# Kernel tuning notes

Hardware: AMD Instinct MI355X
Metric: run time of the kernel (lower is better)

## Reference

```python
import jax, jax.numpy as jnp
import numpy as np

N, E, H, D, FE = 50000, 400000, 4, 64, 64  # nodes, edges, heads, per-head dim, edge feat dim
NEG_SLOPE = 0.2


def setup_inputs() -> dict:
    key = jax.random.key(0)
    ks = jax.random.split(key, 18)
    def p(k, shape, s=0.1):
        return jax.random.normal(k, shape, dtype=jnp.float32) * s
    return dict(
        features=p(ks[0], (N, D), 1.0),
        edge_feat=p(ks[1], (E, FE), 1.0),
        src=jax.random.randint(ks[2], (E,), 0, N),
        dst=jax.random.randint(ks[3], (E,), 0, N),
        # layer 0: in=64 -> H*D=256, residual Linear since 64 != 256
        W0=p(ks[4], (D, H * D)), We0=p(ks[5], (FE, H * D)),
        al0=p(ks[6], (H, D)), ar0=p(ks[7], (H, D)), ae0=p(ks[8], (H, D)),
        b0=p(ks[9], (H * D,)), Wres0=p(ks[10], (D, H * D)),
        # layer 1 (last): in=256 -> H*D=256, residual = identity view
        W1=p(ks[11], (H * D, H * D)), We1=p(ks[12], (FE, H * D)),
        al1=p(ks[13], (H, D)), ar1=p(ks[14], (H, D)), ae1=p(ks[15], (H, D)),
        b1=p(ks[16], (H * D,)),
    )


def _edge_gat_layer(h, ef, src, dst, W, We, al, ar, ae, b, Wres=None):
    n = h.shape[0]
    ft = (h @ W).reshape(n, H, D)          # (N,H,D) projected node feats
    fe = (ef @ We).reshape(-1, H, D)       # (E,H,D) projected edge feats
    el = jnp.sum(ft * al, axis=-1)         # (N,H)
    er = jnp.sum(ft * ar, axis=-1)         # (N,H)
    ee = jnp.sum(fe * ae, axis=-1)         # (E,H)
    e = el[src] + er[dst] + ee             # (E,H)
    e = jnp.where(e > 0, e, NEG_SLOPE * e)  # leaky_relu(0.2)
    # segment softmax over incoming edges of each dst node
    m = jax.ops.segment_max(jax.lax.stop_gradient(e), dst, num_segments=n)
    ex = jnp.exp(e - m[dst])
    den = jax.ops.segment_sum(ex, dst, num_segments=n)
    a = ex / den[dst]                      # (E,H) attention
    out = jax.ops.segment_sum(ft[src] * a[:, :, None], dst, num_segments=n)  # (N,H,D)
    res = (h @ Wres).reshape(n, H, D) if Wres is not None else h.reshape(n, H, D)
    return out + res + b.reshape(1, H, D)


def reference(features, edge_feat, src, dst,
              W0, We0, al0, ar0, ae0, b0, Wres0,
              W1, We1, al1, ar1, ae1, b1):
    h = _edge_gat_layer(features, edge_feat, src, dst, W0, We0, al0, ar0, ae0, b0, Wres0)
    h = jax.nn.elu(h.reshape(N, H * D))    # flatten heads + ELU between layers
    h = _edge_gat_layer(h, edge_feat, src, dst, W1, We1, al1, ar1, ae1, b1)
    return h.mean(axis=1)                  # (N, D) mean over heads on last layer
```

## Files before the change

kernel.cpp:

```cpp
#include <hip/hip_runtime.h>
#include <hip/hip_bf16.h>

#define NN 50000
#define EE 400000
#define NB 196

typedef __bf16 bf16_8 __attribute__((ext_vector_type(8)));
typedef float f32x4 __attribute__((ext_vector_type(4)));

__global__ __launch_bounds__(256) void prep_kernel(
    const float* __restrict__ features, __bf16* __restrict__ fbf,
    const float* __restrict__ W0, const float* __restrict__ Wres0, __bf16* __restrict__ Bt0,
    const float* __restrict__ W1, __bf16* __restrict__ Bt1,
    const float* __restrict__ We0, const float* __restrict__ ae0, float* __restrict__ Ve0,
    const float* __restrict__ We1, const float* __restrict__ ae1, float* __restrict__ Ve1,
    const int* __restrict__ dst, int* __restrict__ cnt) {
  int b = blockIdx.x;
  int t = threadIdx.x;
  if (b < 1563) {
    int i = b * 256 + t;
    if (i < NN * 64 / 8) {
      const float4* p = (const float4*)features + (size_t)i * 2;
      float4 a = p[0], c = p[1];
      bf16_8 v = {(__bf16)a.x, (__bf16)a.y, (__bf16)a.z, (__bf16)a.w,
                  (__bf16)c.x, (__bf16)c.y, (__bf16)c.z, (__bf16)c.w};
      *(bf16_8*)(fbf + (size_t)i * 8) = v;
    }
  } else if (b < 1563 + 128) {
    int idx = (b - 1563) * 256 + t;
    int j = idx >> 6, k = idx & 63;
    float v = (j < 256) ? W0[k * 256 + j] : Wres0[k * 256 + (j - 256)];
    Bt0[idx] = (__bf16)v;
  } else if (b < 1563 + 128 + 256) {
    int idx = (b - 1563 - 128) * 256 + t;
    int j = idx >> 8, k = idx & 255;
    Bt1[idx] = (__bf16)W1[k * 256 + j];
  } else if (b == 1947) {
    int f = t >> 2, h = t & 3;
    float s = 0.f;
    for (int d = 0; d < 64; ++d) s += We0[f * 256 + h * 64 + d] * ae0[h * 64 + d];
    Ve0[f * 4 + h] = s;
  } else if (b == 1948) {
    int f = t >> 2, h = t & 3;
    float s = 0.f;
    for (int d = 0; d < 64; ++d) s += We1[f * 256 + h * 64 + d] * ae1[h * 64 + d];
    Ve1[f * 4 + h] = s;
  } else {
    int e = (b - 1949) * 256 + t;
    if (e < EE) atomicAdd(&cnt[dst[e]], 1);
  }
}

__global__ __launch_bounds__(256) void scan1_kernel(const int* __restrict__ cnt,
                                                    int* __restrict__ scanbuf,
                                                    int* __restrict__ blocksum) {
  __shared__ int s[256];
  int t = threadIdx.x;
  int idx = blockIdx.x * 256 + t;
  int c = (idx < NN) ? cnt[idx] : 0;
  s[t] = c;
  __syncthreads();
  for (int d = 1; d < 256; d <<= 1) {
    int v = (t >= d) ? s[t - d] : 0;
    __syncthreads();
    s[t] += v;
    __syncthreads();
  }
  if (idx < NN) scanbuf[idx] = s[t];
  if (t == 255) blocksum[blockIdx.x] = s[255];
}

__global__ __launch_bounds__(256) void scan2_kernel(const int* __restrict__ blocksum,
                                                    int* __restrict__ blockoff, int nb) {
  __shared__ int s[256];
  int t = threadIdx.x;
  int c = (t < nb) ? blocksum[t] : 0;
  s[t] = c;
  __syncthreads();
  for (int d = 1; d < 256; d <<= 1) {
    int v = (t >= d) ? s[t - d] : 0;
    __syncthreads();
    s[t] += v;
    __syncthreads();
  }
  if (t < nb) blockoff[t] = s[t] - c;
}

__global__ __launch_bounds__(256) void scan3_kernel(const int* __restrict__ scanbuf,
                                                    const int* __restrict__ cnt,
                                                    const int* __restrict__ blockoff,
                                                    int* __restrict__ off,
                                                    int* __restrict__ cur) {
  int idx = blockIdx.x * 256 + threadIdx.x;
  if (idx < NN) {
    int o = blockoff[blockIdx.x] + scanbuf[idx] - cnt[idx];
    off[idx] = o;
    cur[idx] = o;
  }
  if (idx == 0) off[NN] = EE;
}

__global__ __launch_bounds__(256) void fill_kernel(const int* __restrict__ src,
                                                   const int* __restrict__ dst,
                                                   int* __restrict__ cur,
                                                   int* __restrict__ srcc,
                                                   int* __restrict__ eidc) {
  int e = blockIdx.x * 256 + threadIdx.x;
  if (e < EE) {
    int p = atomicAdd(&cur[dst[e]], 1);
    srcc[p] = src[e];
    eidc[p] = e;
  }
}

__global__ __launch_bounds__(256) void eek_kernel(const float* __restrict__ ef,
                                                  const float* __restrict__ Ve0,
                                                  const float* __restrict__ Ve1,
                                                  float* __restrict__ eeo) {
  __shared__ float V0[256], V1[256];
  V0[threadIdx.x] = Ve0[threadIdx.x];
  V1[threadIdx.x] = Ve1[threadIdx.x];
  __syncthreads();
  int r = threadIdx.x >> 2, sub = threadIdx.x & 3;
  int e = blockIdx.x * 64 + r;
  if (e >= EE) return;
  float a0 = 0, a1 = 0, a2 = 0, a3 = 0;
  float c0 = 0, c1 = 0, c2 = 0, c3 = 0;
  const float* row = ef + (size_t)e * 64 + sub * 16;
#pragma unroll
  for (int i = 0; i < 16; i += 4) {
    float4 v = *(const float4*)(row + i);
    float xs[4] = {v.x, v.y, v.z, v.w};
#pragma unroll
    for (int j = 0; j < 4; ++j) {
      float x = xs[j];
      int idx = (sub * 16 + i + j) * 4;
      a0 += x * V0[idx + 0]; a1 += x * V0[idx + 1];
      a2 += x * V0[idx + 2]; a3 += x * V0[idx + 3];
      c0 += x * V1[idx + 0]; c1 += x * V1[idx + 1];
      c2 += x * V1[idx + 2]; c3 += x * V1[idx + 3];
    }
  }
#pragma unroll
  for (int o = 1; o < 4; o <<= 1) {
    a0 += __shfl_xor(a0, o); a1 += __shfl_xor(a1, o);
    a2 += __shfl_xor(a2, o); a3 += __shfl_xor(a3, o);
    c0 += __shfl_xor(c0, o); c1 += __shfl_xor(c1, o);
    c2 += __shfl_xor(c2, o); c3 += __shfl_xor(c3, o);
  }
  if (sub == 0) {
    float4 u; u.x = a0; u.y = a1; u.z = a2; u.w = a3;
    float4 w; w.x = c0; w.y = c1; w.z = c2; w.w = c3;
    *(float4*)(eeo + (size_t)e * 8) = u;
    *(float4*)(eeo + (size_t)e * 8 + 4) = w;
  }
}

#define LDK 40
__global__ __launch_bounds__(256) void gemm_kernel(const __bf16* __restrict__ A,
                                                   const __bf16* __restrict__ Bt,
                                                   __bf16* __restrict__ ft,
                                                   __bf16* __restrict__ base,
                                                   const float* __restrict__ bias,
                                                   const float* __restrict__ al,
                                                   const float* __restrict__ ar,
                                                   float* __restrict__ el,
                                                   float* __restrict__ er,
                                                   int M, int K) {
  __shared__ __align__(16) __bf16 Al[64 * LDK];
  __shared__ __align__(16) __bf16 Bl[64 * LDK];
  int tid = threadIdx.x;
  int wav = tid >> 6, lane = tid & 63;
  int quad = lane >> 4, l16 = lane & 15;
  int bm = blockIdx.x * 64;
  int bn = blockIdx.y * 64;
  int sr = tid >> 2;
  int sk = (tid & 3) << 3;

  f32x4 acc[4] = {{0, 0, 0, 0}, {0, 0, 0, 0}, {0, 0, 0, 0}, {0, 0, 0, 0}};

  for (int k0 = 0; k0 < K; k0 += 32) {
    uint4 av = {0, 0, 0, 0};
    int arow = bm + sr;
    if (arow < M) av = *(const uint4*)(A + (size_t)arow * K + k0 + sk);
    uint4 bv = *(const uint4*)(Bt + (size_t)(bn + sr) * K + k0 + sk);
    __syncthreads();
    *(uint4*)&Al[sr * LDK + sk] = av;
    *(uint4*)&Bl[sr * LDK + sk] = bv;
    __syncthreads();
    bf16_8 af = *(const bf16_8*)&Al[(wav * 16 + l16) * LDK + quad * 8];
#pragma unroll
    for (int nt = 0; nt < 4; ++nt) {
      bf16_8 bf = *(const bf16_8*)&Bl[(nt * 16 + l16) * LDK + quad * 8];
      acc[nt] = __builtin_amdgcn_mfma_f32_16x16x32_bf16(af, bf, acc[nt], 0, 0, 0);
    }
  }

  int row0 = bm + wav * 16 + quad * 4;

  if (bn < 256) {
    int hb = bn >> 6;
#pragma unroll
    for (int r = 0; r < 4; ++r) {
      float pl = 0.f, pr = 0.f;
#pragma unroll
      for (int nt = 0; nt < 4; ++nt) {
        float v = acc[nt][r];
        int d = nt * 16 + l16;
        pl += v * al[hb * 64 + d];
        pr += v * ar[hb * 64 + d];
      }
#pragma unroll
      for (int o2 = 8; o2 > 0; o2 >>= 1) {
        pl += __shfl_xor(pl, o2);
        pr += __shfl_xor(pr, o2);
      }
      int row = row0 + r;
      if (l16 == 0 && row < M) {
        el[row * 4 + hb] = pl;
        er[row * 4 + hb] = pr;
      }
    }
  }

#pragma unroll
  for (int nt = 0; nt < 4; ++nt) {
    int col = bn + nt * 16 + l16;
#pragma unroll
    for (int r = 0; r < 4; ++r) {
      int row = row0 + r;
      if (row < M) {
        float v = acc[nt][r];
        if (col < 256)
          ft[(size_t)row * 256 + col] = (__bf16)v;
        else
          base[(size_t)row * 256 + (col - 256)] = (__bf16)(v + bias[col - 256]);
      }
    }
  }
}

template <int LAYER>
__global__ __launch_bounds__(256) void agg_kernel(const int* __restrict__ off,
                                                  const int* __restrict__ srcc,
                                                  const int* __restrict__ eidc,
                                                  const float* __restrict__ eeo,
                                                  const float* __restrict__ el,
                                                  const float* __restrict__ er,
                                                  const __bf16* __restrict__ ft,
                                                  const __bf16* prev,
                                                  const float* __restrict__ bias,
                                                  __bf16* outb,
                                                  float* __restrict__ outf) {
  __shared__ float red[256];
  int n = blockIdx.x;
  int t = threadIdx.x, h = t >> 6, lane = t & 63;
  int beg = off[n], end = off[n + 1];
  float pv = (float)prev[(size_t)n * 256 + t];
  float bv = (LAYER == 1) ? bias[t] : 0.f;
  float ern = er[n * 4 + h];
  int offd = h * 64 + lane;

  float acc = 0.f, den = 0.f;
  int j = beg;
  for (; j + 4 <= end; j += 4) {
    int s0 = srcc[j], s1 = srcc[j + 1], s2 = srcc[j + 2], s3 = srcc[j + 3];
    int e0 = eidc[j], e1 = eidc[j + 1], e2 = eidc[j + 2], e3 = eidc[j + 3];
    float z0 = el[s0 * 4 + h] + ern + eeo[(size_t)e0 * 8 + LAYER * 4 + h];
    float z1 = el[s1 * 4 + h] + ern + eeo[(size_t)e1 * 8 + LAYER * 4 + h];
    float z2 = el[s2 * 4 + h] + ern + eeo[(size_t)e2 * 8 + LAYER * 4 + h];
    float z3 = el[s3 * 4 + h] + ern + eeo[(size_t)e3 * 8 + LAYER * 4 + h];
    float w0 = __expf(z0 > 0.f ? z0 : 0.2f * z0);
    float w1 = __expf(z1 > 0.f ? z1 : 0.2f * z1);
    float w2 = __expf(z2 > 0.f ? z2 : 0.2f * z2);
    float w3 = __expf(z3 > 0.f ? z3 : 0.2f * z3);
    float v0 = (float)ft[(size_t)s0 * 256 + offd];
    float v1 = (float)ft[(size_t)s1 * 256 + offd];
    float v2 = (float)ft[(size_t)s2 * 256 + offd];
    float v3 = (float)ft[(size_t)s3 * 256 + offd];
    acc += w0 * v0; acc += w1 * v1; acc += w2 * v2; acc += w3 * v3;
    den += w0 + w1 + w2 + w3;
  }
  for (; j < end; ++j) {
    int s = srcc[j];
    float z = el[s * 4 + h] + ern + eeo[(size_t)eidc[j] * 8 + LAYER * 4 + h];
    float w = __expf(z > 0.f ? z : 0.2f * z);
    acc += w * (float)ft[(size_t)s * 256 + offd];
    den += w;
  }
  float res = (end > beg) ? acc / den : 0.f;

  if (LAYER == 0) {
    float v = res + pv;
    v = v > 0.f ? v : (__expf(v) - 1.0f);
    outb[(size_t)n * 256 + t] = (__bf16)v;
  } else {
    red[t] = res + pv + bv;
    __syncthreads();
    if (t < 64)
      outf[(size_t)n * 64 + t] =
          0.25f * (red[t] + red[t + 64] + red[t + 128] + red[t + 192]);
  }
}

extern "C" void kernel_launch(void* const* d_in, const int* in_sizes, int n_in,
                              void* d_out, int out_size, void* d_ws, size_t ws_size,
                              hipStream_t stream) {
  const float* features  = (const float*)d_in[0];
  const float* edge_feat = (const float*)d_in[1];
  const int*   src       = (const int*)d_in[2];
  const int*   dst       = (const int*)d_in[3];
  const float* W0    = (const float*)d_in[4];
  const float* We0   = (const float*)d_in[5];
  const float* al0   = (const float*)d_in[6];
  const float* ar0   = (const float*)d_in[7];
  const float* ae0   = (const float*)d_in[8];
  const float* b0    = (const float*)d_in[9];
  const float* Wres0 = (const float*)d_in[10];
  const float* W1    = (const float*)d_in[11];
  const float* We1   = (const float*)d_in[12];
  const float* al1   = (const float*)d_in[13];
  const float* ar1   = (const float*)d_in[14];
  const float* ae1   = (const float*)d_in[15];
  const float* b1    = (const float*)d_in[16];
  float* out = (float*)d_out;

  char* ws = (char*)d_ws;
  size_t o = 0;
  auto alloc = [&](size_t bytes) {
    void* p = ws + o;
    o = (o + bytes + 255) & ~(size_t)255;
    return p;
  };
  int*    cnt      = (int*)alloc((size_t)NN * 4);
  int*    scanbuf  = (int*)alloc((size_t)NN * 4);
  int*    blocksum = (int*)alloc(256 * 4);
  int*    blockoff = (int*)alloc(256 * 4);
  int*    off      = (int*)alloc((size_t)(NN + 1) * 4);
  int*    cur      = (int*)alloc((size_t)NN * 4);
  int*    srcc     = (int*)alloc((size_t)EE * 4);
  int*    eidc     = (int*)alloc((size_t)EE * 4);
  float*  eeo      = (float*)alloc((size_t)EE * 8 * 4);
  float*  el       = (float*)alloc((size_t)NN * 4 * 4);
  float*  er       = (float*)alloc((size_t)NN * 4 * 4);
  float*  Ve0      = (float*)alloc(256 * 4);
  float*  Ve1      = (float*)alloc(256 * 4);
  __bf16* Bt0      = (__bf16*)alloc((size_t)512 * 64 * 2);
  __bf16* Bt1      = (__bf16*)alloc((size_t)256 * 256 * 2);
  __bf16* fbf      = (__bf16*)alloc((size_t)NN * 64 * 2);
  __bf16* ft       = (__bf16*)alloc((size_t)NN * 256 * 2);
  __bf16* base     = (__bf16*)alloc((size_t)NN * 256 * 2);
  __bf16* h1       = base;

  const int EB = (EE + 255) / 256;
  const int MG = (NN + 63) / 64;

  hipMemsetAsync(cnt, 0, (size_t)NN * 4, stream);
  prep_kernel<<<1949 + EB, 256, 0, stream>>>(features, fbf, W0, Wres0, Bt0, W1, Bt1,
                                             We0, ae0, Ve0, We1, ae1, Ve1, dst, cnt);
  scan1_kernel<<<NB, 256, 0, stream>>>(cnt, scanbuf, blocksum);
  scan2_kernel<<<1, 256, 0, stream>>>(blocksum, blockoff, NB);
  scan3_kernel<<<NB, 256, 0, stream>>>(scanbuf, cnt, blockoff, off, cur);
  fill_kernel<<<EB, 256, 0, stream>>>(src, dst, cur, srcc, eidc);
  eek_kernel<<<(EE + 63) / 64, 256, 0, stream>>>(edge_feat, Ve0, Ve1, eeo);

  gemm_kernel<<<dim3(MG, 8), 256, 0, stream>>>(fbf, Bt0, ft, base, b0, al0, ar0, el, er, NN, 64);
  agg_kernel<0><<<NN, 256, 0, stream>>>(off, srcc, eidc, eeo, el, er, ft, base, nullptr, h1, nullptr);

  gemm_kernel<<<dim3(MG, 4), 256, 0, stream>>>(h1, Bt1, ft, nullptr, nullptr, al1, ar1, el, er, NN, 256);
  agg_kernel<1><<<NN, 256, 0, stream>>>(off, srcc, eidc, eeo, el, er, ft, h1, b1, nullptr, out);
}
```

Measured before the change: 445.8 us.

## Precompute per-edge attention weights in separate kernel and merge scan passes

Adds a wts_kernel that computes the leaky-relu exponentiated attention weight for every CSR-ordered edge once, stored head-major, so the aggregation kernel no longer does redundant per-lane gathers of el, eidc and eeo with repeated exp. A dst-sorted array is written during fill to support this. It also fuses scan2 and scan3 into one kernel where each block reduces the preceding block sums itself, and reorganises the edge-projection kernel so each 16-lane group reads one row with coalesced float4 loads. The cost is an extra kernel per layer and an extra 6.4 MB weight buffer written and read back.

```diff
diff --git a/kernel.cpp b/kernel.cpp
--- a/kernel.cpp
+++ b/kernel.cpp
@@ -70,30 +70,23 @@
   if (t == 255) blocksum[blockIdx.x] = s[255];
 }
 
-__global__ __launch_bounds__(256) void scan2_kernel(const int* __restrict__ blocksum,
-                                                    int* __restrict__ blockoff, int nb) {
+__global__ __launch_bounds__(256) void scan23_kernel(const int* __restrict__ scanbuf,
+                                                     const int* __restrict__ cnt,
+                                                     const int* __restrict__ blocksum,
+                                                     int* __restrict__ off,
+                                                     int* __restrict__ cur) {
   __shared__ int s[256];
-  int t = threadIdx.x;
-  int c = (t < nb) ? blocksum[t] : 0;
-  s[t] = c;
+  int t = threadIdx.x, b = blockIdx.x;
+  s[t] = (t < b) ? blocksum[t] : 0;
   __syncthreads();
-  for (int d = 1; d < 256; d <<= 1) {
-    int v = (t >= d) ? s[t - d] : 0;
-    __syncthreads();
-    s[t] += v;
-    __syncthreads();
-  }
-  if (t < nb) blockoff[t] = s[t] - c;
-}
-
-__global__ __launch_bounds__(256) void scan3_kernel(const int* __restrict__ scanbuf,
-                                                    const int* __restrict__ cnt,
-                                                    const int* __restrict__ blockoff,
-                                                    int* __restrict__ off,
-                                                    int* __restrict__ cur) {
-  int idx = blockIdx.x * 256 + threadIdx.x;
+  for (int d = 128; d > 0; d >>= 1) {
+    if (t < d) s[t] += s[t + d];
+    __syncthreads();
+  }
+  int base = s[0];
+  int idx = b * 256 + t;
   if (idx < NN) {
-    int o = blockoff[blockIdx.x] + scanbuf[idx] - cnt[idx];
+    int o = base + scanbuf[idx] - cnt[idx];
     off[idx] = o;
     cur[idx] = o;
   }
@@ -104,12 +97,15 @@
                                                    const int* __restrict__ dst,
                                                    int* __restrict__ cur,
                                                    int* __restrict__ srcc,
-                                                   int* __restrict__ eidc) {
+                                                   int* __restrict__ eidc,
+                                                   int* __restrict__ dstc) {
   int e = blockIdx.x * 256 + threadIdx.x;
   if (e < EE) {
-    int p = atomicAdd(&cur[dst[e]], 1);
+    int d = dst[e];
+    int p = atomicAdd(&cur[d], 1);
     srcc[p] = src[e];
     eidc[p] = e;
+    dstc[p] = d;
   }
 }
 
@@ -121,38 +117,35 @@
   V0[threadIdx.x] = Ve0[threadIdx.x];
   V1[threadIdx.x] = Ve1[threadIdx.x];
   __syncthreads();
-  int r = threadIdx.x >> 2, sub = threadIdx.x & 3;
-  int e = blockIdx.x * 64 + r;
-  if (e >= EE) return;
-  float a0 = 0, a1 = 0, a2 = 0, a3 = 0;
-  float c0 = 0, c1 = 0, c2 = 0, c3 = 0;
-  const float* row = ef + (size_t)e * 64 + sub * 16;
-#pragma unroll
-  for (int i = 0; i < 16; i += 4) {
-    float4 v = *(const float4*)(row + i);
+  int t = threadIdx.x;
+  int colg = (t & 15) * 4;
+#pragma unroll
+  for (int it = 0; it < 4; ++it) {
+    int e16 = blockIdx.x * 64 + it * 16;
+    float4 v = *(const float4*)(ef + (size_t)e16 * 64 + t * 4);
+    float a[8] = {0, 0, 0, 0, 0, 0, 0, 0};
     float xs[4] = {v.x, v.y, v.z, v.w};
 #pragma unroll
-    for (int j = 0; j < 4; ++j) {
-      float x = xs[j];
-      int idx = (sub * 16 + i + j) * 4;
-      a0 += x * V0[idx + 0]; a1 += x * V0[idx + 1];
-      a2 += x * V0[idx + 2]; a3 += x * V0[idx + 3];
-      c0 += x * V1[idx + 0]; c1 += x * V1[idx + 1];
-      c2 += x * V1[idx + 2]; c3 += x * V1[idx + 3];
-    }
-  }
-#pragma unroll
-  for (int o = 1; o < 4; o <<= 1) {
-    a0 += __shfl_xor(a0, o); a1 += __shfl_xor(a1, o);
-    a2 += __shfl_xor(a2, o); a3 += __shfl_xor(a3, o);
-    c0 += __shfl_xor(c0, o); c1 += __shfl_xor(c1, o);
-    c2 += __shfl_xor(c2, o); c3 += __shfl_xor(c3, o);
-  }
-  if (sub == 0) {
-    float4 u; u.x = a0; u.y = a1; u.z = a2; u.w = a3;
-    float4 w; w.x = c0; w.y = c1; w.z = c2; w.w = c3;
-    *(float4*)(eeo + (size_t)e * 8) = u;
-    *(float4*)(eeo + (size_t)e * 8 + 4) = w;
+    for (int jj = 0; jj < 4; ++jj) {
+      float x = xs[jj];
+      int c4 = (colg + jj) * 4;
+      a[0] += x * V0[c4 + 0]; a[1] += x * V0[c4 + 1];
+      a[2] += x * V0[c4 + 2]; a[3] += x * V0[c4 + 3];
+      a[4] += x * V1[c4 + 0]; a[5] += x * V1[c4 + 1];
+      a[6] += x * V1[c4 + 2]; a[7] += x * V1[c4 + 3];
+    }
+#pragma unroll
+    for (int o = 1; o < 16; o <<= 1) {
+#pragma unroll
+      for (int k = 0; k < 8; ++k) a[k] += __shfl_xor(a[k], o);
+    }
+    if ((t & 15) == 0) {
+      int e = e16 + (t >> 4);
+      float4 u; u.x = a[0]; u.y = a[1]; u.z = a[2]; u.w = a[3];
+      float4 w; w.x = a[4]; w.y = a[5]; w.z = a[6]; w.w = a[7];
+      *(float4*)(eeo + (size_t)e * 8) = u;
+      *(float4*)(eeo + (size_t)e * 8 + 4) = w;
+    }
   }
 }
 
@@ -241,12 +234,34 @@
 }
 
 template <int LAYER>
+__global__ __launch_bounds__(256) void wts_kernel(const int* __restrict__ srcc,
+                                                  const int* __restrict__ dstc,
+                                                  const int* __restrict__ eidc,
+                                                  const float* __restrict__ el,
+                                                  const float* __restrict__ er,
+                                                  const float* __restrict__ eeo,
+                                                  float* __restrict__ wts) {
+  int p = blockIdx.x * 256 + threadIdx.x;
+  if (p >= EE) return;
+  int s = srcc[p], d = dstc[p], e = eidc[p];
+  float4 l = *(const float4*)(el + (size_t)s * 4);
+  float4 r = *(const float4*)(er + (size_t)d * 4);
+  float4 c = *(const float4*)(eeo + (size_t)e * 8 + LAYER * 4);
+  float4 z;
+  z.x = l.x + r.x + c.x;
+  z.y = l.y + r.y + c.y;
+  z.z = l.z + r.z + c.z;
+  z.w = l.w + r.w + c.w;
+  wts[0 * EE + p] = __expf(z.x > 0.f ? z.x : 0.2f * z.x);
+  wts[1 * EE + p] = __expf(z.y > 0.f ? z.y : 0.2f * z.y);
+  wts[2 * EE + p] = __expf(z.z > 0.f ? z.z : 0.2f * z.z);
+  wts[3 * EE + p] = __expf(z.w > 0.f ? z.w : 0.2f * z.w);
+}
+
+template <int LAYER>
 __global__ __launch_bounds__(256) void agg_kernel(const int* __restrict__ off,
                                                   const int* __restrict__ srcc,
-                                                  const int* __restrict__ eidc,
-                                                  const float* __restrict__ eeo,
-                                                  const float* __restrict__ el,
-                                                  const float* __restrict__ er,
+                                                  const float* __restrict__ wts,
                                                   const __bf16* __restrict__ ft,
                                                   const __bf16* prev,
                                                   const float* __restrict__ bias,
@@ -258,34 +273,24 @@
   int beg = off[n], end = off[n + 1];
   float pv = (float)prev[(size_t)n * 256 + t];
   float bv = (LAYER == 1) ? bias[t] : 0.f;
-  float ern = er[n * 4 + h];
-  int offd = h * 64 + lane;
+  const float* wh = wts + (size_t)h * EE;
+  const __bf16* ftp = ft + h * 64 + lane;
 
   float acc = 0.f, den = 0.f;
   int j = beg;
   for (; j + 4 <= end; j += 4) {
     int s0 = srcc[j], s1 = srcc[j + 1], s2 = srcc[j + 2], s3 = srcc[j + 3];
-    int e0 = eidc[j], e1 = eidc[j + 1], e2 = eidc[j + 2], e3 = eidc[j + 3];
-    float z0 = el[s0 * 4 + h] + ern + eeo[(size_t)e0 * 8 + LAYER * 4 + h];
-    float z1 = el[s1 * 4 + h] + ern + eeo[(size_t)e1 * 8 + LAYER * 4 + h];
-    float z2 = el[s2 * 4 + h] + ern + eeo[(size_t)e2 * 8 + LAYER * 4 + h];
-    float z3 = el[s3 * 4 + h] + ern + eeo[(size_t)e3 * 8 + LAYER * 4 + h];
-    float w0 = __expf(z0 > 0.f ? z0 : 0.2f * z0);
-    float w1 = __expf(z1 > 0.f ? z1 : 0.2f * z1);
-    float w2 = __expf(z2 > 0.f ? z2 : 0.2f * z2);
-    float w3 = __expf(z3 > 0.f ? z3 : 0.2f * z3);
-    float v0 = (float)ft[(size_t)s0 * 256 + offd];
-    float v1 = (float)ft[(size_t)s1 * 256 + offd];
-    float v2 = (float)ft[(size_t)s2 * 256 + offd];
-    float v3 = (float)ft[(size_t)s3 * 256 + offd];
+    float w0 = wh[j], w1 = wh[j + 1], w2 = wh[j + 2], w3 = wh[j + 3];
+    float v0 = (float)ftp[(size_t)s0 * 256];
+    float v1 = (float)ftp[(size_t)s1 * 256];
+    float v2 = (float)ftp[(size_t)s2 * 256];
+    float v3 = (float)ftp[(size_t)s3 * 256];
     acc += w0 * v0; acc += w1 * v1; acc += w2 * v2; acc += w3 * v3;
     den += w0 + w1 + w2 + w3;
   }
   for (; j < end; ++j) {
-    int s = srcc[j];
-    float z = el[s * 4 + h] + ern + eeo[(size_t)eidc[j] * 8 + LAYER * 4 + h];
-    float w = __expf(z > 0.f ? z : 0.2f * z);
-    acc += w * (float)ft[(size_t)s * 256 + offd];
+    float w = wh[j];
+    acc += w * (float)ftp[(size_t)srcc[j] * 256];
     den += w;
   }
   float res = (end > beg) ? acc / den : 0.f;
@@ -335,12 +340,13 @@
   int*    cnt      = (int*)alloc((size_t)NN * 4);
   int*    scanbuf  = (int*)alloc((size_t)NN * 4);
   int*    blocksum = (int*)alloc(256 * 4);
-  int*    blockoff = (int*)alloc(256 * 4);
   int*    off      = (int*)alloc((size_t)(NN + 1) * 4);
   int*    cur      = (int*)alloc((size_t)NN * 4);
   int*    srcc     = (int*)alloc((size_t)EE * 4);
   int*    eidc     = (int*)alloc((size_t)EE * 4);
+  int*    dstc     = (int*)alloc((size_t)EE * 4);
   float*  eeo      = (float*)alloc((size_t)EE * 8 * 4);
+  float*  wts      = (float*)alloc((size_t)EE * 4 * 4);
   float*  el       = (float*)alloc((size_t)NN * 4 * 4);
   float*  er       = (float*)alloc((size_t)NN * 4 * 4);
   float*  Ve0      = (float*)alloc(256 * 4);
@@ -359,14 +365,15 @@
   prep_kernel<<<1949 + EB, 256, 0, stream>>>(features, fbf, W0, Wres0, Bt0, W1, Bt1,
                                              We0, ae0, Ve0, We1, ae1, Ve1, dst, cnt);
   scan1_kernel<<<NB, 256, 0, stream>>>(cnt, scanbuf, blocksum);
-  scan2_kernel<<<1, 256, 0, stream>>>(blocksum, blockoff, NB);
-  scan3_kernel<<<NB, 256, 0, stream>>>(scanbuf, cnt, blockoff, off, cur);
-  fill_kernel<<<EB, 256, 0, stream>>>(src, dst, cur, srcc, eidc);
-  eek_kernel<<<(EE + 63) / 64, 256, 0, stream>>>(edge_feat, Ve0, Ve1, eeo);
+  scan23_kernel<<<NB, 256, 0, stream>>>(scanbuf, cnt, blocksum, off, cur);
+  fill_kernel<<<EB, 256, 0, stream>>>(src, dst, cur, srcc, eidc, dstc);
+  eek_kernel<<<EE / 64, 256, 0, stream>>>(edge_feat, Ve0, Ve1, eeo);
 
   gemm_kernel<<<dim3(MG, 8), 256, 0, stream>>>(fbf, Bt0, ft, base, b0, al0, ar0, el, er, NN, 64);
-  agg_kernel<0><<<NN, 256, 0, stream>>>(off, srcc, eidc, eeo, el, er, ft, base, nullptr, h1, nullptr);
+  wts_kernel<0><<<EB, 256, 0, stream>>>(srcc, dstc, eidc, el, er, eeo, wts);
+  agg_kernel<0><<<NN, 256, 0, stream>>>(off, srcc, wts, ft, base, nullptr, h1, nullptr);
 
   gemm_kernel<<<dim3(MG, 4), 256, 0, stream>>>(h1, Bt1, ft, nullptr, nullptr, al1, ar1, el, er, NN, 256);
-  agg_kernel<1><<<NN, 256, 0, stream>>>(off, srcc, eidc, eeo, el, er, ft, h1, b1, nullptr, out);
-}
+  wts_kernel<1><<<EB, 256, 0, stream>>>(srcc, dstc, eidc, el, er, eeo, wts);
+  agg_kernel<1><<<NN, 256, 0, stream>>>(off, srcc, wts, ft, h1, b1, nullptr, out);
+}
```

Result: slower. 460.6 us (+3.3%).
